# Kernel optimization log

Hardware: AMD Instinct MI355X
Metric: run time of the kernel (lower is better)

Reference implementation:

```python
import jax, jax.numpy as jnp
import numpy as np

ROI, P = 28, 7          # ROI window on feature map; output grid 7x7 -> 4x4 bins
BIN = ROI // P
C, CLASSES = 64, 2      # channels after vgg features[:2]; n classes
H = W = 512
N_ROI = 2000
D_FC = 4096


def setup_inputs() -> dict:
    key = jax.random.key(0)
    k = jax.random.split(key, 8)
    s = 0.02
    return {
        "img": jax.random.normal(k[0], (3, H, W), jnp.float32),
        "regions": jax.random.randint(k[1], (N_ROI, 2), 0, H - ROI, jnp.int32),
        "conv_w": jax.random.normal(k[2], (C, 3, 3, 3), jnp.float32) * s,
        "conv_b": jnp.zeros((C,), jnp.float32),
        "fc1_w": jax.random.normal(k[3], (D_FC, C * P * P), jnp.float32) * s,
        "fc1_b": jnp.zeros((D_FC,), jnp.float32),
        "fc2_w": jax.random.normal(k[4], (D_FC, D_FC), jnp.float32) * s,
        "fc2_b": jnp.zeros((D_FC,), jnp.float32),
        "cls_w": jax.random.normal(k[5], (CLASSES, D_FC), jnp.float32) * s,
        "cls_b": jnp.zeros((CLASSES,), jnp.float32),
        "bbox_w": jax.random.normal(k[6], (CLASSES * 4, D_FC), jnp.float32) * s,
        "bbox_b": jnp.zeros((CLASSES * 4,), jnp.float32),
    }


def reference(img, regions, conv_w, conv_b, fc1_w, fc1_b,
              fc2_w, fc2_b, cls_w, cls_b, bbox_w, bbox_b):
    # conv trunk: vgg16.features[:2] = Conv2d(3,64,3,pad=1) + ReLU
    fmap = jax.lax.conv_general_dilated(
        img[None], conv_w, window_strides=(1, 1), padding="SAME",
        dimension_numbers=("NCHW", "OIHW", "NCHW"))[0]
    fmap = jax.nn.relu(fmap + conv_b[:, None, None])        # [C, H, W]

    # per-region crop (irregular gather), vectorized over regions
    def crop(rc):
        return jax.lax.dynamic_slice(fmap, (0, rc[0], rc[1]), (C, ROI, ROI))
    rois = jax.vmap(crop)(regions)                          # [N, C, ROI, ROI]

    # RoI max pooling: divide ROIxROI window into PxP grid, max each bin
    pooled = rois.reshape(N_ROI, C, P, BIN, P, BIN).max(axis=(3, 5))  # [N,C,P,P]
    feat = pooled.reshape(N_ROI, C * P * P)

    # vgg classifier[:-1] (Dropout = identity at inference)
    feat = jax.nn.relu(feat @ fc1_w.T + fc1_b)
    feat = jax.nn.relu(feat @ fc2_w.T + fc2_b)              # [N, 4096]

    cls_logits = feat @ cls_w.T + cls_b                     # [N, CLASSES]
    loc_bbox = feat @ bbox_w.T + bbox_b                     # [N, CLASSES*4]
    return (cls_logits, loc_bbox)
```

## Files before the change

kernel.cpp:

```cpp
#include <hip/hip_runtime.h>

typedef unsigned short u16;
typedef unsigned int u32;
using bf16x8 = __attribute__((ext_vector_type(8))) short;
using f32x4  = __attribute__((ext_vector_type(4))) float;
using ushort8 = __attribute__((ext_vector_type(8))) unsigned short;

__device__ __forceinline__ u16 f2bf(float f) {
  u32 u = __float_as_uint(f);
  return (u16)((u + 0x7FFFu + ((u >> 16) & 1u)) >> 16);
}
__device__ __forceinline__ float bf2f(u16 h) {
  return __uint_as_float(((u32)h) << 16);
}
__device__ __forceinline__ ushort8 umax8(ushort8 a, ushort8 b) {
  return __builtin_elementwise_max(a, b);
}

__global__ __launch_bounds__(512) void conv_vmax_k(
    const float* __restrict__ img, const float* __restrict__ w,
    const float* __restrict__ bias, u16* __restrict__ M1) {
  const int t = threadIdx.x;
  const int x = ((blockIdx.x & 15) << 5) + (t >> 4);
  const int cq = (t & 15) << 2;
  const int y0 = (blockIdx.x >> 4) << 3;

  float wr[27][4];
#pragma unroll
  for (int p = 0; p < 27; ++p)
#pragma unroll
    for (int c = 0; c < 4; ++c) wr[p][c] = w[(cq + c) * 27 + p];
  float bz[4];
#pragma unroll
  for (int c = 0; c < 4; ++c) bz[c] = bias[cq + c];

  const bool xm = (x > 0), xp = (x < 511);
  float win[3][3][3];

#define LOADROW(yy, s)                                                        \
  do {                                                                        \
    if ((yy) >= 0 && (yy) <= 511) {                                          \
      _Pragma("unroll") for (int ci = 0; ci < 3; ++ci) {                      \
        const float* rp = img + ci * 262144 + (yy) * 512 + x;                 \
        win[ci][s][0] = xm ? rp[-1] : 0.f;                                    \
        win[ci][s][1] = rp[0];                                                \
        win[ci][s][2] = xp ? rp[1] : 0.f;                                     \
      }                                                                        \
    } else {                                                                   \
      _Pragma("unroll") for (int ci = 0; ci < 3; ++ci) {                      \
        win[ci][s][0] = 0.f; win[ci][s][1] = 0.f; win[ci][s][2] = 0.f;        \
      }                                                                        \
    }                                                                          \
  } while (0)

  LOADROW(y0 - 1, 0);
  LOADROW(y0, 1);

  float h0[4], h1[4], h2[4], cur[4];
#pragma unroll
  for (int i = 0; i < 11; ++i) {
    const int r = y0 + i;
    LOADROW(r + 1, 2);
    if (r <= 511) {
#pragma unroll
      for (int c = 0; c < 4; ++c) cur[c] = bz[c];
#pragma unroll
      for (int ci = 0; ci < 3; ++ci)
#pragma unroll
        for (int ky = 0; ky < 3; ++ky)
#pragma unroll
          for (int kx = 0; kx < 3; ++kx) {
            const float iv = win[ci][ky][kx];
            const int p = ci * 9 + ky * 3 + kx;
#pragma unroll
            for (int c = 0; c < 4; ++c) cur[c] = fmaf(wr[p][c], iv, cur[c]);
          }
#pragma unroll
      for (int c = 0; c < 4; ++c) cur[c] = fmaxf(cur[c], 0.f);
    } else {
#pragma unroll
      for (int c = 0; c < 4; ++c) cur[c] = 0.f;
    }
    if (i >= 3) {
      const int ym = r - 3;
      float m[4];
#pragma unroll
      for (int c = 0; c < 4; ++c)
        m[c] = fmaxf(fmaxf(h0[c], h1[c]), fmaxf(h2[c], cur[c]));
      uint2 o;
      o.x = (u32)f2bf(m[0]) | ((u32)f2bf(m[1]) << 16);
      o.y = (u32)f2bf(m[2]) | ((u32)f2bf(m[3]) << 16);
      *(uint2*)(M1 + (((size_t)(ym * 512 + x)) << 6) + cq) = o;
    }
#pragma unroll
    for (int c = 0; c < 4; ++c) { h0[c] = h1[c]; h1[c] = h2[c]; h2[c] = cur[c]; }
#pragma unroll
    for (int ci = 0; ci < 3; ++ci)
#pragma unroll
      for (int kx = 0; kx < 3; ++kx) {
        win[ci][0][kx] = win[ci][1][kx];
        win[ci][1][kx] = win[ci][2][kx];
      }
  }
#undef LOADROW
}

__global__ __launch_bounds__(256) void roipool2_k(
    const u16* __restrict__ M1, const int* __restrict__ regions,
    u16* __restrict__ feat) {
  int n = blockIdx.x, t = threadIdx.x;
  uint4* fdst = (uint4*)(feat + (size_t)n * 3136);
  if (n >= 2000) {
    uint4 z; z.x = z.y = z.z = z.w = 0u;
    for (int w = t; w < 392; w += 256) fdst[w] = z;
    return;
  }
  __shared__ u16 frow[3136];
  int r0 = regions[2 * n], c0 = regions[2 * n + 1];
  for (int w = t; w < 392; w += 256) {
    int bin = w >> 3, cg = w & 7;
    int py = bin / 7, px = bin % 7;
    int y = r0 + py * 4, xb = c0 + px * 4;
    const u16* base = M1 + (((size_t)(y * 512 + xb)) << 6) + cg * 8;
    ushort8 a = *(const ushort8*)(base);
    ushort8 b = *(const ushort8*)(base + 64);
    ushort8 c = *(const ushort8*)(base + 128);
    ushort8 d = *(const ushort8*)(base + 192);
    ushort8 m = umax8(umax8(a, b), umax8(c, d));
#pragma unroll
    for (int k = 0; k < 8; ++k) frow[(cg * 8 + k) * 49 + bin] = m[k];
  }
  __syncthreads();
  const uint4* fsrc = (const uint4*)frow;
  for (int w = t; w < 392; w += 256) fdst[w] = fsrc[w];
}

__global__ __launch_bounds__(256) void f2bf2_k(
    const float* __restrict__ in1, u16* __restrict__ out1, int n4a,
    const float* __restrict__ in2, u16* __restrict__ out2, int n4total) {
  int idx = blockIdx.x * 256 + threadIdx.x;
  int stride = gridDim.x * 256;
  for (int i = idx; i < n4total; i += stride) {
    const float* in; u16* o16; int k;
    if (i < n4a) { in = in1; o16 = out1; k = i; }
    else         { in = in2; o16 = out2; k = i - n4a; }
    float4 v = ((const float4*)in)[k];
    uint2 o;
    o.x = (u32)f2bf(v.x) | ((u32)f2bf(v.y) << 16);
    o.y = (u32)f2bf(v.z) | ((u32)f2bf(v.w) << 16);
    ((uint2*)o16)[k] = o;
  }
}

__global__ __launch_bounds__(512, 2) void gemm8_bt_relu_k(
    const u16* __restrict__ A, const u16* __restrict__ B,
    const float* __restrict__ bias, u16* __restrict__ C, int N, int K) {
  __shared__ uint4 lds4[9216];
  char* ldsb = (char*)lds4;
  const int t = threadIdx.x;
  const int lane = t & 63, wv = t >> 6;
  const int wm = wv >> 2, wn = wv & 3;

  int bid = blockIdx.x;
  int swz = ((bid & 7) << 5) | (bid >> 3);
  const int nb = swz >> 4, mb = swz & 15;
  const int m0 = mb * 128, n0 = nb * 256;

  const u16* __restrict__ Ab = A + (size_t)m0 * K;
  const u16* __restrict__ Bb = B + (size_t)n0 * K;

  const int srow = t >> 3;
  const int sslot = (t & 7) ^ (srow & 7);
  const u16* pA0 = Ab + (size_t)srow * K + sslot * 8;
  const u16* pA1 = pA0 + (size_t)64 * K;
  const u16* pB0 = Bb + (size_t)srow * K + sslot * 8;
  const u16* pB1 = pB0 + (size_t)64 * K;
  const u16* pB2 = pB0 + (size_t)128 * K;
  const u16* pB3 = pB0 + (size_t)192 * K;
  const int dof = t * 16;

#define G2L(src, ldst)                                                        \
  __builtin_amdgcn_global_load_lds(                                          \
      (const __attribute__((address_space(1))) void*)(src),                  \
      (__attribute__((address_space(3))) void*)(ldst), 16, 0, 0)

  const int rA = wm * 64 + (lane & 15);
  const int rB = wn * 64 + (lane & 15);
  const int sl = lane >> 4;
#define LOFF(r, slot) (((r) << 7) + ((((slot) ^ ((r) & 7))) << 4))

  f32x4 acc[4][4] = {};
  bf16x8 afr[4][2], bfr[4][2];

  const int NT = K >> 6;
  {
    char* A0 = ldsb; char* B0 = A0 + 16384;
    char* A1 = ldsb + 49152; char* B1 = A1 + 16384;
    G2L(pA0, A0 + dof); G2L(pA1, A0 + 8192 + dof);
    G2L(pB0, B0 + dof); G2L(pB1, B0 + 8192 + dof);
    G2L(pB2, B0 + 16384 + dof); G2L(pB3, B0 + 24576 + dof);
    G2L(pA0 + 64, A1 + dof); G2L(pA1 + 64, A1 + 8192 + dof);
    G2L(pB0 + 64, B1 + dof); G2L(pB1 + 64, B1 + 8192 + dof);
    G2L(pB2 + 64, B1 + 16384 + dof); G2L(pB3 + 64, B1 + 24576 + dof);
  }
  asm volatile("s_waitcnt vmcnt(6)" ::: "memory");
  __builtin_amdgcn_s_barrier();

  int cb = 0;
  for (int tt = 0; tt < NT; ++tt) {
    const int pb = (cb + 2 >= 3) ? cb - 1 : cb + 2;
    const bool pf = (tt + 2) < NT;
    char* Acur = ldsb + cb * 49152; char* Bcur = Acur + 16384;
    char* Apf  = ldsb + pb * 49152; char* Bpf  = Apf + 16384;
    const int kof = (tt + 2) << 6;

    if (pf) {
      G2L(pA0 + kof, Apf + dof);
      G2L(pA1 + kof, Apf + 8192 + dof);
      G2L(pB0 + kof, Bpf + dof);
      G2L(pB1 + kof, Bpf + 8192 + dof);
      G2L(pB2 + kof, Bpf + 16384 + dof);
      G2L(pB3 + kof, Bpf + 24576 + dof);
    }
    __builtin_amdgcn_sched_barrier(0);
    __builtin_amdgcn_s_setprio(1);
#pragma unroll
    for (int j = 0; j < 4; ++j) {
      bfr[j][0] = *(const bf16x8*)(Bcur + LOFF(rB + j * 16, sl));
      bfr[j][1] = *(const bf16x8*)(Bcur + LOFF(rB + j * 16, 4 + sl));
    }
#pragma unroll
    for (int i = 0; i < 4; ++i) {
      afr[i][0] = *(const bf16x8*)(Acur + LOFF(rA + i * 16, sl));
      afr[i][1] = *(const bf16x8*)(Acur + LOFF(rA + i * 16, 4 + sl));
    }
#pragma unroll
    for (int i = 0; i < 4; ++i)
#pragma unroll
      for (int j = 0; j < 4; ++j) {
        acc[i][j] = __builtin_amdgcn_mfma_f32_16x16x32_bf16(afr[i][0], bfr[j][0], acc[i][j], 0, 0, 0);
        acc[i][j] = __builtin_amdgcn_mfma_f32_16x16x32_bf16(afr[i][1], bfr[j][1], acc[i][j], 0, 0, 0);
      }
    __builtin_amdgcn_s_setprio(0);
    if (pf) {
      asm volatile("s_waitcnt vmcnt(6)" ::: "memory");
    } else if (tt + 1 < NT) {
      asm volatile("s_waitcnt vmcnt(0)" ::: "memory");
    }
    __builtin_amdgcn_s_barrier();
    cb = (cb == 2) ? 0 : cb + 1;
  }
#undef G2L
#undef LOFF

  float bv[4];
#pragma unroll
  for (int j = 0; j < 4; ++j) bv[j] = bias[n0 + wn * 64 + j * 16 + (lane & 15)];
#pragma unroll
  for (int i = 0; i < 4; ++i)
#pragma unroll
    for (int j = 0; j < 4; ++j) {
      int cg = n0 + wn * 64 + j * 16 + (lane & 15);
#pragma unroll
      for (int r = 0; r < 4; ++r) {
        int rg = m0 + wm * 64 + i * 16 + (lane >> 4) * 4 + r;
        float v = fmaxf(acc[i][j][r] + bv[j], 0.f);
        C[(size_t)rg * N + cg] = f2bf(v);
      }
    }
}

__global__ __launch_bounds__(256) void heads_k(
    const u16* __restrict__ h2, const float* __restrict__ cw,
    const float* __restrict__ cb, const float* __restrict__ bw,
    const float* __restrict__ bb, float* __restrict__ out) {
  __shared__ u16 wl[10][4096];
  __shared__ float red[4][10];
  const int t = threadIdx.x;
  for (int i4 = t; i4 < 10240; i4 += 256) {
    int j = i4 >> 10, k4 = i4 & 1023;
    float4 v = (j < 2) ? ((const float4*)cw)[j * 1024 + k4]
                       : ((const float4*)bw)[(j - 2) * 1024 + k4];
    uint2 o;
    o.x = (u32)f2bf(v.x) | ((u32)f2bf(v.y) << 16);
    o.y = (u32)f2bf(v.z) | ((u32)f2bf(v.w) << 16);
    *(uint2*)(&wl[j][k4 * 4]) = o;
  }
  __syncthreads();
  const int lane = t & 63, wvi = t >> 6;
  const int m0 = blockIdx.x * 8;
  for (int mi = 0; mi < 8; ++mi) {
    const int m = m0 + mi;
    const u16* hrow = h2 + (size_t)m * 4096;
    float p[10];
#pragma unroll
    for (int j = 0; j < 10; ++j) p[j] = 0.f;
#pragma unroll
    for (int h = 0; h < 2; ++h) {
      const int kc = t + h * 256;
      ushort8 hv = ((const ushort8*)hrow)[kc];
      float hf[8];
#pragma unroll
      for (int e = 0; e < 8; ++e) hf[e] = bf2f(hv[e]);
#pragma unroll
      for (int j = 0; j < 10; ++j) {
        ushort8 wv = *(const ushort8*)(&wl[j][kc * 8]);
#pragma unroll
        for (int e = 0; e < 8; ++e) p[j] = fmaf(hf[e], bf2f(wv[e]), p[j]);
      }
    }
#pragma unroll
    for (int j = 0; j < 10; ++j)
#pragma unroll
      for (int off = 32; off > 0; off >>= 1) p[j] += __shfl_down(p[j], off);
    if (lane == 0) {
#pragma unroll
      for (int j = 0; j < 10; ++j) red[wvi][j] = p[j];
    }
    __syncthreads();
    if (t < 10) {
      float s = red[0][t] + red[1][t] + red[2][t] + red[3][t];
      s += (t < 2) ? cb[t] : bb[t - 2];
      if (t < 2) out[m * 2 + t] = s;
      else out[4000 + m * 8 + (t - 2)] = s;
    }
    __syncthreads();
  }
}

extern "C" void kernel_launch(void* const* d_in, const int* in_sizes, int n_in,
                              void* d_out, int out_size, void* d_ws, size_t ws_size,
                              hipStream_t stream) {
  const float* img    = (const float*)d_in[0];
  const int*   regions= (const int*)d_in[1];
  const float* conv_w = (const float*)d_in[2];
  const float* conv_b = (const float*)d_in[3];
  const float* fc1_w  = (const float*)d_in[4];
  const float* fc1_b  = (const float*)d_in[5];
  const float* fc2_w  = (const float*)d_in[6];
  const float* fc2_b  = (const float*)d_in[7];
  const float* cls_w  = (const float*)d_in[8];
  const float* cls_b  = (const float*)d_in[9];
  const float* bbox_w = (const float*)d_in[10];
  const float* bbox_b = (const float*)d_in[11];
  float* out = (float*)d_out;

  char* ws = (char*)d_ws;
  u16* M1   = (u16*)(ws);
  u16* h1   = (u16*)(ws);
  u16* h2   = (u16*)(ws + 16777216);
  u16* feat = (u16*)(ws + 33554432);
  u16* w1b  = (u16*)(ws + 46399488);
  u16* w2b  = (u16*)(ws + 72089600);

  conv_vmax_k<<<1024, 512, 0, stream>>>(img, conv_w, conv_b, M1);
  roipool2_k<<<2048, 256, 0, stream>>>(M1, regions, feat);
  f2bf2_k<<<2048, 256, 0, stream>>>(fc1_w, w1b, 3211264, fc2_w, w2b, 7405568);
  gemm8_bt_relu_k<<<256, 512, 0, stream>>>(feat, w1b, fc1_b, h1, 4096, 3136);
  gemm8_bt_relu_k<<<256, 512, 0, stream>>>(h1, w2b, fc2_b, h2, 4096, 4096);
  heads_k<<<250, 256, 0, stream>>>(h2, cls_w, cls_b, bbox_w, bbox_b, out);
}
```

Before: 222.7 us.

## Fuse fp32-to-bf16 weight conversion into GEMM B-tile loading

Removes the separate weight conversion kernel and has each GEMM load fp32 weight rows through registers. It converts them to bf16 and writes them into swizzled LDS, double-buffered across iterations. This avoids a full write and re-read of the converted weights and one launch. In exchange, each M-block re-reads and re-converts fp32 weights, doubling weight bytes fetched. Register pressure also rises from the staged float4 buffers.

```diff
diff --git a/kernel.cpp b/kernel.cpp
--- a/kernel.cpp
+++ b/kernel.cpp
@@ -135,25 +135,8 @@
   for (int w = t; w < 392; w += 256) fdst[w] = fsrc[w];
 }
 
-__global__ __launch_bounds__(256) void f2bf2_k(
-    const float* __restrict__ in1, u16* __restrict__ out1, int n4a,
-    const float* __restrict__ in2, u16* __restrict__ out2, int n4total) {
-  int idx = blockIdx.x * 256 + threadIdx.x;
-  int stride = gridDim.x * 256;
-  for (int i = idx; i < n4total; i += stride) {
-    const float* in; u16* o16; int k;
-    if (i < n4a) { in = in1; o16 = out1; k = i; }
-    else         { in = in2; o16 = out2; k = i - n4a; }
-    float4 v = ((const float4*)in)[k];
-    uint2 o;
-    o.x = (u32)f2bf(v.x) | ((u32)f2bf(v.y) << 16);
-    o.y = (u32)f2bf(v.z) | ((u32)f2bf(v.w) << 16);
-    ((uint2*)o16)[k] = o;
-  }
-}
-
-__global__ __launch_bounds__(512, 2) void gemm8_bt_relu_k(
-    const u16* __restrict__ A, const u16* __restrict__ B,
+__global__ __launch_bounds__(512, 2) void gemm8_fw_relu_k(
+    const u16* __restrict__ A, const float* __restrict__ Bf,
     const float* __restrict__ bias, u16* __restrict__ C, int N, int K) {
   __shared__ uint4 lds4[9216];
   char* ldsb = (char*)lds4;
@@ -167,89 +150,119 @@
   const int m0 = mb * 128, n0 = nb * 256;
 
   const u16* __restrict__ Ab = A + (size_t)m0 * K;
-  const u16* __restrict__ Bb = B + (size_t)n0 * K;
-
   const int srow = t >> 3;
   const int sslot = (t & 7) ^ (srow & 7);
   const u16* pA0 = Ab + (size_t)srow * K + sslot * 8;
   const u16* pA1 = pA0 + (size_t)64 * K;
-  const u16* pB0 = Bb + (size_t)srow * K + sslot * 8;
-  const u16* pB1 = pB0 + (size_t)64 * K;
-  const u16* pB2 = pB0 + (size_t)128 * K;
-  const u16* pB3 = pB0 + (size_t)192 * K;
   const int dof = t * 16;
+
+  const int brow = t >> 1, bhalf = t & 1;
+  const float* __restrict__ pBf = Bf + (size_t)(n0 + brow) * K + bhalf * 32;
+  int bwoff[4];
+#pragma unroll
+  for (int q = 0; q < 4; ++q)
+    bwoff[q] = 16384 + (brow << 7) + ((((bhalf << 2) + q) ^ (brow & 7)) << 4);
 
 #define G2L(src, ldst)                                                        \
   __builtin_amdgcn_global_load_lds(                                          \
       (const __attribute__((address_space(1))) void*)(src),                  \
       (__attribute__((address_space(3))) void*)(ldst), 16, 0, 0)
+#define LOFF(r, slot) (((r) << 7) + ((((slot) ^ ((r) & 7))) << 4))
+
+#define BLOAD(S, koff)                                                        \
+  _Pragma("unroll") for (int q = 0; q < 8; ++q)                               \
+      S[q] = *(const float4*)(pBf + (koff) + q * 4);
+
+#define BCVTW(S, bufb)                                                        \
+  do {                                                                        \
+    _Pragma("unroll") for (int q = 0; q < 4; ++q) {                           \
+      uint4 Wq;                                                               \
+      Wq.x = (u32)f2bf(S[2 * q].x) | ((u32)f2bf(S[2 * q].y) << 16);           \
+      Wq.y = (u32)f2bf(S[2 * q].z) | ((u32)f2bf(S[2 * q].w) << 16);           \
+      Wq.z = (u32)f2bf(S[2 * q + 1].x) | ((u32)f2bf(S[2 * q + 1].y) << 16);   \
+      Wq.w = (u32)f2bf(S[2 * q + 1].z) | ((u32)f2bf(S[2 * q + 1].w) << 16);   \
+      *(uint4*)((bufb) + bwoff[q]) = Wq;                                      \
+    }                                                                         \
+  } while (0)
 
   const int rA = wm * 64 + (lane & 15);
   const int rB = wn * 64 + (lane & 15);
   const int sl = lane >> 4;
-#define LOFF(r, slot) (((r) << 7) + ((((slot) ^ ((r) & 7))) << 4))
 
   f32x4 acc[4][4] = {};
   bf16x8 afr[4][2], bfr[4][2];
+  float4 sE[8], sO[8];
 
   const int NT = K >> 6;
   {
-    char* A0 = ldsb; char* B0 = A0 + 16384;
-    char* A1 = ldsb + 49152; char* B1 = A1 + 16384;
-    G2L(pA0, A0 + dof); G2L(pA1, A0 + 8192 + dof);
-    G2L(pB0, B0 + dof); G2L(pB1, B0 + 8192 + dof);
-    G2L(pB2, B0 + 16384 + dof); G2L(pB3, B0 + 24576 + dof);
-    G2L(pA0 + 64, A1 + dof); G2L(pA1 + 64, A1 + 8192 + dof);
-    G2L(pB0 + 64, B1 + dof); G2L(pB1 + 64, B1 + 8192 + dof);
-    G2L(pB2 + 64, B1 + 16384 + dof); G2L(pB3 + 64, B1 + 24576 + dof);
-  }
-  asm volatile("s_waitcnt vmcnt(6)" ::: "memory");
-  __builtin_amdgcn_s_barrier();
+    char* b0 = ldsb;
+    char* b1 = ldsb + 49152;
+    BLOAD(sE, 0);
+    G2L(pA0, b0 + dof); G2L(pA1, b0 + 8192 + dof);
+    BLOAD(sO, 64);
+    G2L(pA0 + 64, b1 + dof); G2L(pA1 + 64, b1 + 8192 + dof);
+    asm volatile("s_waitcnt vmcnt(12)" ::: "memory");
+    BCVTW(sE, b0);
+    asm volatile("s_waitcnt lgkmcnt(0)" ::: "memory");
+    __builtin_amdgcn_s_barrier();
+  }
+
+#define GBODY(TT, CB, SI, SW)                                                 \
+  do {                                                                        \
+    const bool pf1 = (TT + 1) < NT, pf2 = (TT + 2) < NT;                      \
+    char* cbuf = ldsb + (CB) * 49152;                                         \
+    const int nb3 = ((CB) + 1 == 3) ? 0 : (CB) + 1;                           \
+    const int pb3 = (nb3 + 1 == 3) ? 0 : nb3 + 1;                             \
+    char* wbuf = ldsb + nb3 * 49152;                                          \
+    char* fbuf = ldsb + pb3 * 49152;                                          \
+    const int kof = (TT + 2) << 6;                                            \
+    if (pf2) {                                                                \
+      BLOAD(SI, kof);                                                         \
+      G2L(pA0 + kof, fbuf + dof);                                             \
+      G2L(pA1 + kof, fbuf + 8192 + dof);                                      \
+      asm volatile("s_waitcnt vmcnt(10)" ::: "memory");                       \
+    } else {                                                                  \
+      asm volatile("s_waitcnt vmcnt(0)" ::: "memory");                        \
+    }                                                                         \
+    if (pf1) BCVTW(SW, wbuf);                                                 \
+    __builtin_amdgcn_sched_barrier(0);                                        \
+    __builtin_amdgcn_s_setprio(1);                                            \
+    char* Bcur = cbuf + 16384;                                                \
+    _Pragma("unroll") for (int j = 0; j < 4; ++j) {                           \
+      bfr[j][0] = *(const bf16x8*)(Bcur + LOFF(rB + j * 16, sl));             \
+      bfr[j][1] = *(const bf16x8*)(Bcur + LOFF(rB + j * 16, 4 + sl));         \
+    }                                                                         \
+    _Pragma("unroll") for (int i = 0; i < 4; ++i) {                           \
+      afr[i][0] = *(const bf16x8*)(cbuf + LOFF(rA + i * 16, sl));             \
+      afr[i][1] = *(const bf16x8*)(cbuf + LOFF(rA + i * 16, 4 + sl));         \
+    }                                                                         \
+    _Pragma("unroll") for (int i = 0; i < 4; ++i)                             \
+        _Pragma("unroll") for (int j = 0; j < 4; ++j) {                       \
+      acc[i][j] = __builtin_amdgcn_mfma_f32_16x16x32_bf16(                    \
+          afr[i][0], bfr[j][0], acc[i][j], 0, 0, 0);                          \
+      acc[i][j] = __builtin_amdgcn_mfma_f32_16x16x32_bf16(                    \
+          afr[i][1], bfr[j][1], acc[i][j], 0, 0, 0);                          \
+    }                                                                         \
+    __builtin_amdgcn_s_setprio(0);                                            \
+    asm volatile("s_waitcnt lgkmcnt(0)" ::: "memory");                        \
+    __builtin_amdgcn_s_barrier();                                             \
+  } while (0)
 
   int cb = 0;
-  for (int tt = 0; tt < NT; ++tt) {
-    const int pb = (cb + 2 >= 3) ? cb - 1 : cb + 2;
-    const bool pf = (tt + 2) < NT;
-    char* Acur = ldsb + cb * 49152; char* Bcur = Acur + 16384;
-    char* Apf  = ldsb + pb * 49152; char* Bpf  = Apf + 16384;
-    const int kof = (tt + 2) << 6;
-
-    if (pf) {
-      G2L(pA0 + kof, Apf + dof);
-      G2L(pA1 + kof, Apf + 8192 + dof);
-      G2L(pB0 + kof, Bpf + dof);
-      G2L(pB1 + kof, Bpf + 8192 + dof);
-      G2L(pB2 + kof, Bpf + 16384 + dof);
-      G2L(pB3 + kof, Bpf + 24576 + dof);
-    }
-    __builtin_amdgcn_sched_barrier(0);
-    __builtin_amdgcn_s_setprio(1);
-#pragma unroll
-    for (int j = 0; j < 4; ++j) {
-      bfr[j][0] = *(const bf16x8*)(Bcur + LOFF(rB + j * 16, sl));
-      bfr[j][1] = *(const bf16x8*)(Bcur + LOFF(rB + j * 16, 4 + sl));
-    }
-#pragma unroll
-    for (int i = 0; i < 4; ++i) {
-      afr[i][0] = *(const bf16x8*)(Acur + LOFF(rA + i * 16, sl));
-      afr[i][1] = *(const bf16x8*)(Acur + LOFF(rA + i * 16, 4 + sl));
-    }
-#pragma unroll
-    for (int i = 0; i < 4; ++i)
-#pragma unroll
-      for (int j = 0; j < 4; ++j) {
-        acc[i][j] = __builtin_amdgcn_mfma_f32_16x16x32_bf16(afr[i][0], bfr[j][0], acc[i][j], 0, 0, 0);
-        acc[i][j] = __builtin_amdgcn_mfma_f32_16x16x32_bf16(afr[i][1], bfr[j][1], acc[i][j], 0, 0, 0);
-      }
-    __builtin_amdgcn_s_setprio(0);
-    if (pf) {
-      asm volatile("s_waitcnt vmcnt(6)" ::: "memory");
-    } else if (tt + 1 < NT) {
-      asm volatile("s_waitcnt vmcnt(0)" ::: "memory");
-    }
-    __builtin_amdgcn_s_barrier();
-    cb = (cb == 2) ? 0 : cb + 1;
-  }
+  int tt = 0;
+  for (; tt + 1 < NT; tt += 2) {
+    const int cb0 = cb;
+    const int cb1 = (cb0 + 1 == 3) ? 0 : cb0 + 1;
+    GBODY(tt, cb0, sE, sO);
+    GBODY(tt + 1, cb1, sO, sE);
+    cb = (cb1 + 1 == 3) ? 0 : cb1 + 1;
+  }
+  if (tt < NT) {
+    GBODY(tt, cb, sE, sO);
+  }
+#undef GBODY
+#undef BCVTW
+#undef BLOAD
 #undef G2L
 #undef LOFF
 
@@ -350,13 +363,10 @@
   u16* h1   = (u16*)(ws);
   u16* h2   = (u16*)(ws + 16777216);
   u16* feat = (u16*)(ws + 33554432);
-  u16* w1b  = (u16*)(ws + 46399488);
-  u16* w2b  = (u16*)(ws + 72089600);
 
   conv_vmax_k<<<1024, 512, 0, stream>>>(img, conv_w, conv_b, M1);
   roipool2_k<<<2048, 256, 0, stream>>>(M1, regions, feat);
-  f2bf2_k<<<2048, 256, 0, stream>>>(fc1_w, w1b, 3211264, fc2_w, w2b, 7405568);
-  gemm8_bt_relu_k<<<256, 512, 0, stream>>>(feat, w1b, fc1_b, h1, 4096, 3136);
-  gemm8_bt_relu_k<<<256, 512, 0, stream>>>(h1, w2b, fc2_b, h2, 4096, 4096);
+  gemm8_fw_relu_k<<<256, 512, 0, stream>>>(feat, fc1_w, fc1_b, h1, 4096, 3136);
+  gemm8_fw_relu_k<<<256, 512, 0, stream>>>(h1, fc2_w, fc2_b, h2, 4096, 4096);
   heads_k<<<250, 256, 0, stream>>>(h2, cls_w, cls_b, bbox_w, bbox_b, out);
 }
```

New measurement: 432.0 us. 94.0% more time.

## Fold weight bf16 conversion into conv and roipool kernels as extra blocks

Applied to the files above, without the earlier changes.

Removes the standalone fp32-to-bf16 weight conversion kernel. The fc1 weight conversion now runs as extra blocks appended to the conv kernel, and the fc2 weight conversion runs as extra blocks appended to the roipool kernel. This saves one launch and lets the memory-bound conversion overlap with compute-light conv and roipool work. In exchange, those kernels get larger grids, and the added blocks compete with them for bandwidth and CU slots.

```diff
diff --git a/kernel.cpp b/kernel.cpp
--- a/kernel.cpp
+++ b/kernel.cpp
@@ -16,11 +16,25 @@
 __device__ __forceinline__ ushort8 umax8(ushort8 a, ushort8 b) {
   return __builtin_elementwise_max(a, b);
 }
+__device__ __forceinline__ void cvt_chunk(const float* __restrict__ in,
+                                          u16* __restrict__ out, int i) {
+  float4 v = ((const float4*)in)[i];
+  uint2 o;
+  o.x = (u32)f2bf(v.x) | ((u32)f2bf(v.y) << 16);
+  o.y = (u32)f2bf(v.z) | ((u32)f2bf(v.w) << 16);
+  ((uint2*)out)[i] = o;
+}
 
 __global__ __launch_bounds__(512) void conv_vmax_k(
     const float* __restrict__ img, const float* __restrict__ w,
-    const float* __restrict__ bias, u16* __restrict__ M1) {
+    const float* __restrict__ bias, u16* __restrict__ M1,
+    const float* __restrict__ w1f, u16* __restrict__ w1b) {
   const int t = threadIdx.x;
+  if (blockIdx.x >= 1024) {
+    int idx = (blockIdx.x - 1024) * 512 + t;
+    for (int i = idx; i < 3211264; i += 262144) cvt_chunk(w1f, w1b, i);
+    return;
+  }
   const int x = ((blockIdx.x & 15) << 5) + (t >> 4);
   const int cq = (t & 15) << 2;
   const int y0 = (blockIdx.x >> 4) << 3;
@@ -107,8 +121,14 @@
 
 __global__ __launch_bounds__(256) void roipool2_k(
     const u16* __restrict__ M1, const int* __restrict__ regions,
-    u16* __restrict__ feat) {
+    u16* __restrict__ feat, const float* __restrict__ w2f,
+    u16* __restrict__ w2b) {
   int n = blockIdx.x, t = threadIdx.x;
+  if (n >= 2048) {
+    int idx = (n - 2048) * 256 + t;
+    for (int i = idx; i < 4194304; i += 131072) cvt_chunk(w2f, w2b, i);
+    return;
+  }
   uint4* fdst = (uint4*)(feat + (size_t)n * 3136);
   if (n >= 2000) {
     uint4 z; z.x = z.y = z.z = z.w = 0u;
@@ -133,23 +153,6 @@
   __syncthreads();
   const uint4* fsrc = (const uint4*)frow;
   for (int w = t; w < 392; w += 256) fdst[w] = fsrc[w];
-}
-
-__global__ __launch_bounds__(256) void f2bf2_k(
-    const float* __restrict__ in1, u16* __restrict__ out1, int n4a,
-    const float* __restrict__ in2, u16* __restrict__ out2, int n4total) {
-  int idx = blockIdx.x * 256 + threadIdx.x;
-  int stride = gridDim.x * 256;
-  for (int i = idx; i < n4total; i += stride) {
-    const float* in; u16* o16; int k;
-    if (i < n4a) { in = in1; o16 = out1; k = i; }
-    else         { in = in2; o16 = out2; k = i - n4a; }
-    float4 v = ((const float4*)in)[k];
-    uint2 o;
-    o.x = (u32)f2bf(v.x) | ((u32)f2bf(v.y) << 16);
-    o.y = (u32)f2bf(v.z) | ((u32)f2bf(v.w) << 16);
-    ((uint2*)o16)[k] = o;
-  }
 }
 
 __global__ __launch_bounds__(512, 2) void gemm8_bt_relu_k(
@@ -353,9 +356,8 @@
   u16* w1b  = (u16*)(ws + 46399488);
   u16* w2b  = (u16*)(ws + 72089600);
 
-  conv_vmax_k<<<1024, 512, 0, stream>>>(img, conv_w, conv_b, M1);
-  roipool2_k<<<2048, 256, 0, stream>>>(M1, regions, feat);
-  f2bf2_k<<<2048, 256, 0, stream>>>(fc1_w, w1b, 3211264, fc2_w, w2b, 7405568);
+  conv_vmax_k<<<1536, 512, 0, stream>>>(img, conv_w, conv_b, M1, fc1_w, w1b);
+  roipool2_k<<<2560, 256, 0, stream>>>(M1, regions, feat, fc2_w, w2b);
   gemm8_bt_relu_k<<<256, 512, 0, stream>>>(feat, w1b, fc1_b, h1, 4096, 3136);
   gemm8_bt_relu_k<<<256, 512, 0, stream>>>(h1, w2b, fc2_b, h2, 4096, 4096);
   heads_k<<<250, 256, 0, stream>>>(h2, cls_w, cls_b, bbox_w, bbox_b, out);
```

Result: no change. 219.6 us, median of 4 (-1.4%).
